# Kernel optimization log

Measured on AMD Instinct MI355X. Metric: run time of the kernel, lower is better.

The kernel has to match this reference:

```python
import jax, jax.numpy as jnp
import numpy as np
from jax import lax

NPOINT = 1024
NSAMPLE = 32
EPS = 1e-5


def setup_inputs() -> dict:
    key = jax.random.key(0)
    ks = jax.random.split(key, 8)
    B, N, CF = 16, 4096, 64
    xyz = jax.random.normal(ks[0], (B, N, 3), jnp.float32)
    points = jax.random.normal(ks[1], (B, N, CF), jnp.float32)
    in_ch = 3 + CF
    # 1x1 Conv2d weights stored as (out_ch, in_ch); kaiming-ish scale
    w0 = jax.random.normal(ks[2], (64, in_ch), jnp.float32) / np.sqrt(in_ch)
    w1 = jax.random.normal(ks[3], (64, 64), jnp.float32) / np.sqrt(64)
    w2 = jax.random.normal(ks[4], (128, 64), jnp.float32) / np.sqrt(64)
    z64 = jnp.zeros((64,), jnp.float32)
    z128 = jnp.zeros((128,), jnp.float32)
    o64 = jnp.ones((64,), jnp.float32)
    o128 = jnp.ones((128,), jnp.float32)
    return {
        "xyz": xyz, "points": points,
        "w0": w0, "b0": z64, "g0": o64, "bb0": z64,
        "w1": w1, "b1": z64, "g1": o64, "bb1": z64,
        "w2": w2, "b2": z128, "g2": o128, "bb2": z128,
    }


def _fps(xyz, npoint):
    """Iterative farthest point sampling. xyz: (B,N,3) -> (B,npoint) int32.
    Deterministic start at index 0 (torch uses a random start)."""
    B, N, _ = xyz.shape

    def step(carry, _):
        distance, farthest = carry
        centroid = jnp.take_along_axis(xyz, farthest[:, None, None], axis=1)  # (B,1,3)
        dist = jnp.sum((xyz - centroid) ** 2, -1)  # (B,N)
        distance = jnp.minimum(distance, dist)
        new_far = jnp.argmax(distance, axis=-1).astype(jnp.int32)
        return (distance, new_far), farthest

    init = (jnp.full((B, N), 1e10, xyz.dtype), jnp.zeros((B,), jnp.int32))
    _, cents = lax.scan(step, init, None, length=npoint)  # (npoint, B)
    return cents.T  # (B, npoint)


def _gather(pts, idx):
    """pts: (B,N,C), idx: (B,S,K) -> (B,S,K,C)"""
    return jax.vmap(lambda p, i: p[i])(pts, idx)


def _bn_relu(x, g, b):
    # training-mode BatchNorm over all axes except channel (last), biased var
    mean = jnp.mean(x, axis=(0, 1, 2))
    var = jnp.var(x, axis=(0, 1, 2))
    return jax.nn.relu(g * (x - mean) * lax.rsqrt(var + EPS) + b)


def reference(xyz, points, w0, b0, g0, bb0, w1, b1, g1, bb1, w2, b2, g2, bb2):
    B, N, _ = xyz.shape
    fps_idx = _fps(xyz, NPOINT)  # (B,S)
    new_xyz = jnp.take_along_axis(xyz, fps_idx[..., None], axis=1)  # (B,S,3)
    # squared distances centroid->all points: (B,S,N)
    d2 = (jnp.sum(new_xyz ** 2, -1)[:, :, None]
          + jnp.sum(xyz ** 2, -1)[:, None, :]
          - 2.0 * jnp.einsum("bsc,bnc->bsn", new_xyz, xyz))
    _, idx = lax.top_k(-d2, NSAMPLE)  # (B,S,K) nearest-K (sort-based ball query)
    grouped_xyz = _gather(xyz, idx) - new_xyz[:, :, None, :]  # (B,S,K,3)
    grouped_pts = _gather(points, idx)  # (B,S,K,CF)
    h = jnp.concatenate([grouped_xyz, grouped_pts], axis=-1)  # (B,S,K,3+CF)
    for w, b, g, bb in ((w0, b0, g0, bb0), (w1, b1, g1, bb1), (w2, b2, g2, bb2)):
        h = _bn_relu(jnp.einsum("bskc,oc->bsko", h, w) + b, g, bb)
    new_points = jnp.max(h, axis=2)  # (B,S,C_out) max over K
    new_points = jnp.transpose(new_points, (0, 2, 1))  # (B,C_out,S) matches torch
    return new_xyz, new_points
```

## Files before the change

kernel.cpp:

```cpp
#include <hip/hip_runtime.h>
#include <hip/hip_bf16.h>

#define NB 16
#define NN 4096
#define NS 1024
#define NK 32
#define CF 64
#define CIN 67
#define MTOT 524288
#define NEWP_OFF 49152

__device__ inline void stY(float* p, float v) { *p = v; }
__device__ inline void stY(__hip_bfloat16* p, float v) { *p = __float2bfloat16(v); }
__device__ inline float ldY(const float* p) { return *p; }
__device__ inline float ldY(const __hip_bfloat16* p) { return __bfloat162float(*p); }
__device__ inline float4 ldY4(const float* p) { return *(const float4*)p; }
__device__ inline float4 ldY4(const __hip_bfloat16* p) {
    return make_float4(ldY(p), ldY(p + 1), ldY(p + 2), ldY(p + 3));
}
__device__ inline void stY4(float* p, float4 v) { *(float4*)p = v; }
__device__ inline void stY4(__hip_bfloat16* p, float4 v) {
    stY(p, v.x); stY(p + 1, v.y); stY(p + 2, v.z); stY(p + 3, v.w);
}

template <int CTRL>
__device__ inline float dppredmax(float v) {
    int j = __builtin_amdgcn_update_dpp(__float_as_int(v), __float_as_int(v),
                                        CTRL, 0xF, 0xF, false);
    return fmaxf(v, __int_as_float(j));
}
template <int CTRL>
__device__ inline float dppredmin(float v) {
    int j = __builtin_amdgcn_update_dpp(__float_as_int(v), __float_as_int(v),
                                        CTRL, 0xF, 0xF, false);
    return fminf(v, __int_as_float(j));
}
template <int CTRL>
__device__ inline float dppadd0(float v) {
    int j = __builtin_amdgcn_update_dpp(0, __float_as_int(v), CTRL, 0xF, 0xF, true);
    return __fadd_rn(v, __int_as_float(j));
}
template <int CTRL>
__device__ inline unsigned long long dppredmin64(unsigned long long v) {
    int lo = (int)(unsigned)(v & 0xffffffffULL), hi = (int)(unsigned)(v >> 32);
    unsigned nlo = (unsigned)__builtin_amdgcn_update_dpp(lo, lo, CTRL, 0xF, 0xF, false);
    unsigned nhi = (unsigned)__builtin_amdgcn_update_dpp(hi, hi, CTRL, 0xF, 0xF, false);
    unsigned long long o = ((unsigned long long)nhi << 32) | nlo;
    return o < v ? o : v;
}
__device__ inline float wavemax_to_all(float tmax) {
    float g = tmax;
    g = dppredmax<0x111>(g);
    g = dppredmax<0x112>(g);
    g = dppredmax<0x114>(g);
    g = dppredmax<0x118>(g);
    g = dppredmax<0x142>(g);
    g = dppredmax<0x143>(g);
    return __int_as_float(__builtin_amdgcn_readlane(__float_as_int(g), 63));
}
__device__ inline unsigned long long wavemin64_to_all(unsigned long long v) {
    v = dppredmin64<0x111>(v);
    v = dppredmin64<0x112>(v);
    v = dppredmin64<0x114>(v);
    v = dppredmin64<0x118>(v);
    v = dppredmin64<0x142>(v);
    v = dppredmin64<0x143>(v);
    unsigned lo = (unsigned)__builtin_amdgcn_readlane((int)(unsigned)(v & 0xffffffffULL), 63);
    unsigned hi = (unsigned)__builtin_amdgcn_readlane((int)(unsigned)(v >> 32), 63);
    return ((unsigned long long)hi << 32) | lo;
}
__device__ inline float segsum16(float v) {
    v = dppadd0<0x111>(v); v = dppadd0<0x112>(v);
    v = dppadd0<0x114>(v); v = dppadd0<0x118>(v);
    return v;
}
__device__ inline float segsum32(float v) {
    v = segsum16(v); v = dppadd0<0x142>(v);
    return v;
}
__device__ inline float quadmax(float v) {
    v = dppredmax<0xB1>(v); v = dppredmax<0x4E>(v);
    return v;
}
__device__ inline float quadmin(float v) {
    v = dppredmin<0xB1>(v); v = dppredmin<0x4E>(v);
    return v;
}

__global__ __launch_bounds__(256) void fps_kernel(const float* __restrict__ xyz,
                                                  int* __restrict__ fps_idx) {
    __shared__ float4 cpt[NN];
    __shared__ unsigned long long part[2][4];
    const int b = blockIdx.x, t = threadIdx.x;
    const float4* src = (const float4*)(xyz + (size_t)b * NN * 3);
    float px[16], py[16], pz[16], dist[16];
#pragma unroll
    for (int j = 0; j < 4; ++j) {
        float4 A = src[t * 12 + 3 * j], B4 = src[t * 12 + 3 * j + 1], C4 = src[t * 12 + 3 * j + 2];
        px[4 * j + 0] = A.x;  py[4 * j + 0] = A.y;  pz[4 * j + 0] = A.z;
        px[4 * j + 1] = A.w;  py[4 * j + 1] = B4.x; pz[4 * j + 1] = B4.y;
        px[4 * j + 2] = B4.z; py[4 * j + 2] = B4.w; pz[4 * j + 2] = C4.x;
        px[4 * j + 3] = C4.y; py[4 * j + 3] = C4.z; pz[4 * j + 3] = C4.w;
    }
#pragma unroll
    for (int i = 0; i < 16; ++i) {
        dist[i] = 1e10f;
        cpt[16 * t + i] = make_float4(px[i], py[i], pz[i], 0.f);
    }
    __syncthreads();
    int cur = 0;
    float4 c = cpt[0];
    const int wv = t >> 6;
    for (int s = 0; s < NS; ++s) {
        if (t == 0) fps_idx[(b << 10) + s] = cur;
#pragma unroll
        for (int i = 0; i < 16; ++i) {
            float dx = __fsub_rn(px[i], c.x), dy = __fsub_rn(py[i], c.y), dz = __fsub_rn(pz[i], c.z);
            float d = __fadd_rn(__fadd_rn(__fmul_rn(dx, dx), __fmul_rn(dy, dy)), __fmul_rn(dz, dz));
            dist[i] = fminf(dist[i], d);
        }
        float m0 = fmaxf(dist[0], dist[1]),   m1 = fmaxf(dist[2], dist[3]);
        float m2 = fmaxf(dist[4], dist[5]),   m3 = fmaxf(dist[6], dist[7]);
        float m4 = fmaxf(dist[8], dist[9]),   m5 = fmaxf(dist[10], dist[11]);
        float m6 = fmaxf(dist[12], dist[13]), m7 = fmaxf(dist[14], dist[15]);
        m0 = fmaxf(m0, m1); m2 = fmaxf(m2, m3); m4 = fmaxf(m4, m5); m6 = fmaxf(m6, m7);
        m0 = fmaxf(m0, m2); m4 = fmaxf(m4, m6);
        const float tmax = fmaxf(m0, m4);
        int mi = 15;
#pragma unroll
        for (int i = 14; i >= 0; --i) mi = (dist[i] == tmax) ? i : mi;
        const float gmax = wavemax_to_all(tmax);
        unsigned long long mask = __ballot(tmax == gmax);
        int ldr = __ffsll(mask) - 1;
        int widx = __builtin_amdgcn_readlane(16 * t + mi, ldr);
        if ((t & 63) == 0) {
            part[s & 1][wv] =
                ((unsigned long long)__float_as_uint(gmax) << 32) | (unsigned)(4095 - widx);
        }
        __syncthreads();
        unsigned long long k0 = part[s & 1][0], k1 = part[s & 1][1];
        unsigned long long k2 = part[s & 1][2], k3 = part[s & 1][3];
        unsigned long long ka = k0 > k1 ? k0 : k1, kb = k2 > k3 ? k2 : k3;
        unsigned long long k = ka > kb ? ka : kb;
        cur = 4095 - (int)(unsigned)(k & 0xffffffffu);
        c = cpt[cur];
    }
}

__global__ __launch_bounds__(256) void knn_kernel(const float* __restrict__ xyz,
                                                  const int* __restrict__ fps_idx,
                                                  int* __restrict__ knn,
                                                  float* __restrict__ out) {
    __shared__ float4 cpt[NN];
    const int b = blockIdx.x >> 5, cb = blockIdx.x & 31, t = threadIdx.x;
    for (int p = t; p < NN; p += 256) {
        const float* xr = xyz + ((size_t)(b << 12) + p) * 3;
        float x = xr[0], y = xr[1], z = xr[2];
        float pn = __fadd_rn(__fadd_rn(__fmul_rn(x, x), __fmul_rn(y, y)), __fmul_rn(z, z));
        cpt[p] = make_float4(x, y, z, pn);
    }
    __syncthreads();
    const int lane = t & 63, wv = t >> 6;
    for (int r = 0; r < 8; ++r) {
        const int s = (cb << 5) + (wv << 3) + r;
        const int ci = fps_idx[(b << 10) + s];
        const float4 cq = cpt[ci];
        const float cx = cq.x, cy = cq.y, cz = cq.z, cn = cq.w;
        if (lane < 3) out[((size_t)(b << 10) + s) * 3 + lane] = (lane == 0) ? cx : (lane == 1 ? cy : cz);
        unsigned long long m1 = ~0ULL, m2 = ~0ULL, m3 = ~0ULL;
#pragma unroll
        for (int i = 0; i < 64; ++i) {
            int p = lane + (i << 6);
            float4 q = cpt[p];
            float dot = __fadd_rn(__fadd_rn(__fmul_rn(cx, q.x), __fmul_rn(cy, q.y)),
                                  __fmul_rn(cz, q.z));
            float d2 = __fsub_rn(__fadd_rn(cn, q.w), __fmul_rn(2.0f, dot));
            unsigned u = __float_as_uint(d2);
            unsigned enc = u ^ ((unsigned)((int)u >> 31) | 0x80000000u);
            unsigned long long key = ((unsigned long long)enc << 32) | (unsigned)p;
            if (key < m3) {
                if (key < m1)      { m3 = m2; m2 = m1; m1 = key; }
                else if (key < m2) { m3 = m2; m2 = key; }
                else               { m3 = key; }
            }
        }
        unsigned myidx = 0;
        for (int j = 0; j < 32; ++j) {
            const unsigned long long vmin = wavemin64_to_all(m1);
            if (lane == j) myidx = (unsigned)(vmin & 0xffffffffu);
            if (m1 == vmin) {
                m1 = m2; m2 = m3; m3 = ~0ULL;
                if (m1 == ~0ULL) {
#pragma unroll
                    for (int i = 0; i < 64; ++i) {
                        int p = lane + (i << 6);
                        float4 q = cpt[p];
                        float dot = __fadd_rn(__fadd_rn(__fmul_rn(cx, q.x), __fmul_rn(cy, q.y)),
                                              __fmul_rn(cz, q.z));
                        float d2 = __fsub_rn(__fadd_rn(cn, q.w), __fmul_rn(2.0f, dot));
                        unsigned u = __float_as_uint(d2);
                        unsigned enc = u ^ ((unsigned)((int)u >> 31) | 0x80000000u);
                        unsigned long long key = ((unsigned long long)enc << 32) | (unsigned)p;
                        if (key > vmin && key < m3) {
                            if (key < m1)      { m3 = m2; m2 = m1; m1 = key; }
                            else if (key < m2) { m3 = m2; m2 = key; }
                            else               { m3 = key; }
                        }
                    }
                }
            }
        }
        const int rowbase = ((b << 10) + s) << 5;
        if (lane < 32) knn[rowbase + lane] = (int)myidx;
    }
}

template <typename YT>
__global__ __launch_bounds__(256) void conv0_kernel(
    const float* __restrict__ xyz, const float* __restrict__ points,
    const float* __restrict__ out_xyz, const int* __restrict__ knn,
    const float* __restrict__ w0, const float* __restrict__ b0,
    YT* __restrict__ Y0, float* __restrict__ gs, float* __restrict__ gq) {
    __shared__ float Ht[CIN][128];
    __shared__ float Wt[CIN][64];
    __shared__ float bsm[64], bqm[64];
    const int t = threadIdx.x;
    const int eb = blockIdx.x << 7;
    for (int i = t; i < CIN * 64; i += 256) {
        int c = i >> 6, o = i & 63;
        Wt[c][o] = w0[o * CIN + c];
    }
    {
        const int le = t >> 1, part = t & 1;
        const int e = eb + le;
        const int b = e >> 15, s = (e >> 5) & 1023;
        const int pidx = knn[e];
        const float4* pr = (const float4*)(points + (((size_t)(b << 12) + pidx) << 6)) + (part << 3);
        if (part == 0) {
            const float* xr = xyz + ((size_t)(b << 12) + pidx) * 3;
            const float* cr = out_xyz + ((size_t)(b << 10) + s) * 3;
            Ht[0][le] = xr[0] - cr[0];
            Ht[1][le] = xr[1] - cr[1];
            Ht[2][le] = xr[2] - cr[2];
        }
#pragma unroll
        for (int q = 0; q < 8; ++q) {
            float4 v = pr[q];
            int c = 3 + (part << 5) + (q << 2);
            Ht[c][le] = v.x; Ht[c + 1][le] = v.y; Ht[c + 2][le] = v.z; Ht[c + 3][le] = v.w;
        }
    }
    __syncthreads();
    const int te = t & 31, to = t >> 5;
    float acc[4][8];
#pragma unroll
    for (int j = 0; j < 4; ++j)
#pragma unroll
        for (int i = 0; i < 8; ++i) acc[j][i] = 0.f;
#pragma unroll 2
    for (int c = 0; c < CIN; ++c) {
        const float4 a0 = *(const float4*)&Ht[c][te << 2];
        const float4 wa = *(const float4*)&Wt[c][to << 3];
        const float4 wb = *(const float4*)&Wt[c][(to << 3) + 4];
        const float av[4] = {a0.x, a0.y, a0.z, a0.w};
        const float wvv[8] = {wa.x, wa.y, wa.z, wa.w, wb.x, wb.y, wb.z, wb.w};
#pragma unroll
        for (int j = 0; j < 4; ++j)
#pragma unroll
            for (int i = 0; i < 8; ++i) acc[j][i] += av[j] * wvv[i];
    }
    const int o0 = to << 3;
    float s1v[8], s2v[8];
#pragma unroll
    for (int i = 0; i < 8; ++i) {
        const float bi = b0[o0 + i];
        float ss = 0.f, qq = 0.f;
#pragma unroll
        for (int j = 0; j < 4; ++j) {
            float v = acc[j][i] + bi;
            acc[j][i] = v;
            ss += v; qq += v * v;
        }
        s1v[i] = ss; s2v[i] = qq;
    }
#pragma unroll
    for (int i = 0; i < 8; ++i) {
        const size_t base = (size_t)(o0 + i) * MTOT + eb + (te << 2);
        stY4(&Y0[base], make_float4(acc[0][i], acc[1][i], acc[2][i], acc[3][i]));
    }
#pragma unroll
    for (int i = 0; i < 8; ++i) { s1v[i] = segsum32(s1v[i]); s2v[i] = segsum32(s2v[i]); }
    if ((t & 31) == 31) {
#pragma unroll
        for (int i = 0; i < 8; ++i) { bsm[o0 + i] = s1v[i]; bqm[o0 + i] = s2v[i]; }
    }
    __syncthreads();
    if (t < 64) atomicAdd(&gs[t], bsm[t]);
    else if (t < 128) atomicAdd(&gq[t - 64], bqm[t - 64]);
}

template <typename YT>
__global__ __launch_bounds__(256) void conv1_kernel(
    const YT* __restrict__ Y0, const float* __restrict__ w1, const float* __restrict__ b1,
    const float* __restrict__ gsp, const float* __restrict__ gqp,
    const float* __restrict__ g, const float* __restrict__ bb,
    YT* __restrict__ Y1, float* __restrict__ gs, float* __restrict__ gq) {
    __shared__ float At[64][128];
    __shared__ float Wt[64][64];
    __shared__ float bnsc[64], bnsh[64];
    __shared__ float bsm[64], bqm[64];
    const int t = threadIdx.x;
    const int eb = blockIdx.x << 7;
    if (t < 64) {
        const float inv = 1.f / (float)MTOT;
        float mean = gsp[t] * inv;
        float var = gqp[t] * inv - mean * mean;
        float r = g[t] / sqrtf(var + 1e-5f);
        bnsc[t] = r; bnsh[t] = bb[t] - mean * r;
    }
    for (int i = t; i < 4096; i += 256) {
        int c = i >> 6, o = i & 63;
        Wt[c][o] = w1[o * 64 + c];
    }
    __syncthreads();
#pragma unroll
    for (int r = 0; r < 8; ++r) {
        int L = (r << 8) + t;
        int c = L >> 5, col = (L & 31) << 2;
        float4 y = ldY4(&Y0[(size_t)c * MTOT + eb + col]);
        float sx = bnsc[c], hx = bnsh[c];
        At[c][col]     = fmaxf(sx * y.x + hx, 0.f);
        At[c][col + 1] = fmaxf(sx * y.y + hx, 0.f);
        At[c][col + 2] = fmaxf(sx * y.z + hx, 0.f);
        At[c][col + 3] = fmaxf(sx * y.w + hx, 0.f);
    }
    __syncthreads();
    const int te = t & 15, to = t >> 4;
    float acc[8][4];
#pragma unroll
    for (int j = 0; j < 8; ++j)
#pragma unroll
        for (int i = 0; i < 4; ++i) acc[j][i] = 0.f;
#pragma unroll 2
    for (int c = 0; c < 64; ++c) {
        const float4 a0 = *(const float4*)&At[c][te << 3];
        const float4 a1 = *(const float4*)&At[c][(te << 3) + 4];
        const float4 wa = *(const float4*)&Wt[c][to << 2];
        const float av[8] = {a0.x, a0.y, a0.z, a0.w, a1.x, a1.y, a1.z, a1.w};
        const float wvv[4] = {wa.x, wa.y, wa.z, wa.w};
#pragma unroll
        for (int j = 0; j < 8; ++j)
#pragma unroll
            for (int i = 0; i < 4; ++i) acc[j][i] += av[j] * wvv[i];
    }
    const int o0 = to << 2;
    float s1v[4], s2v[4];
#pragma unroll
    for (int i = 0; i < 4; ++i) {
        const float bi = b1[o0 + i];
        float ss = 0.f, qq = 0.f;
#pragma unroll
        for (int j = 0; j < 8; ++j) {
            float v = acc[j][i] + bi;
            acc[j][i] = v;
            ss += v; qq += v * v;
        }
        s1v[i] = ss; s2v[i] = qq;
    }
#pragma unroll
    for (int i = 0; i < 4; ++i) {
        const size_t base = (size_t)(o0 + i) * MTOT + eb + (te << 3);
        stY4(&Y1[base],     make_float4(acc[0][i], acc[1][i], acc[2][i], acc[3][i]));
        stY4(&Y1[base + 4], make_float4(acc[4][i], acc[5][i], acc[6][i], acc[7][i]));
    }
#pragma unroll
    for (int i = 0; i < 4; ++i) { s1v[i] = segsum16(s1v[i]); s2v[i] = segsum16(s2v[i]); }
    if ((t & 15) == 15) {
#pragma unroll
        for (int i = 0; i < 4; ++i) { bsm[o0 + i] = s1v[i]; bqm[o0 + i] = s2v[i]; }
    }
    __syncthreads();
    if (t < 64) atomicAdd(&gs[t], bsm[t]);
    else if (t < 128) atomicAdd(&gq[t - 64], bqm[t - 64]);
}

template <typename YT>
__global__ __launch_bounds__(256) void conv2s_kernel(
    const YT* __restrict__ Y1, const float* __restrict__ w2, const float* __restrict__ b2,
    const float* __restrict__ gsp, const float* __restrict__ gqp,
    const float* __restrict__ g, const float* __restrict__ bb,
    float* __restrict__ gs, float* __restrict__ gq,
    float* __restrict__ Mx, float* __restrict__ Mn) {
    __shared__ float At[64][128];
    __shared__ float Wt[64][128];
    __shared__ float bnsc[64], bnsh[64];
    __shared__ float bsm[128], bqm[128];
    __shared__ float mxs[4][128], mns[4][128];
    const int t = threadIdx.x;
    const int eb = blockIdx.x << 7;
    if (t < 64) {
        const float inv = 1.f / (float)MTOT;
        float mean = gsp[t] * inv;
        float var = gqp[t] * inv - mean * mean;
        float r = g[t] / sqrtf(var + 1e-5f);
        bnsc[t] = r; bnsh[t] = bb[t] - mean * r;
    }
    for (int i = t; i < 8192; i += 256) {
        int o = i & 127, c = i >> 7;
        Wt[c][o] = w2[o * 64 + c];
    }
    __syncthreads();
#pragma unroll
    for (int r = 0; r < 8; ++r) {
        int L = (r << 8) + t;
        int c = L >> 5, col = (L & 31) << 2;
        float4 y = ldY4(&Y1[(size_t)c * MTOT + eb + col]);
        float sx = bnsc[c], hx = bnsh[c];
        At[c][col]     = fmaxf(sx * y.x + hx, 0.f);
        At[c][col + 1] = fmaxf(sx * y.y + hx, 0.f);
        At[c][col + 2] = fmaxf(sx * y.z + hx, 0.f);
        At[c][col + 3] = fmaxf(sx * y.w + hx, 0.f);
    }
    __syncthreads();
    const int te = t & 15, to = t >> 4;
    float acc[8][8];
#pragma unroll
    for (int j = 0; j < 8; ++j)
#pragma unroll
        for (int i = 0; i < 8; ++i) acc[j][i] = 0.f;
#pragma unroll 2
    for (int c = 0; c < 64; ++c) {
        const float4 a0 = *(const float4*)&At[c][te << 3];
        const float4 a1 = *(const float4*)&At[c][(te << 3) + 4];
        const float4 wa = *(const float4*)&Wt[c][to << 3];
        const float4 wb = *(const float4*)&Wt[c][(to << 3) + 4];
        const float av[8] = {a0.x, a0.y, a0.z, a0.w, a1.x, a1.y, a1.z, a1.w};
        const float wvv[8] = {wa.x, wa.y, wa.z, wa.w, wb.x, wb.y, wb.z, wb.w};
#pragma unroll
        for (int j = 0; j < 8; ++j)
#pragma unroll
            for (int i = 0; i < 8; ++i) acc[j][i] += av[j] * wvv[i];
    }
    const int o0 = to << 3;
    float s1v[8], s2v[8], mxv[8], mnv[8];
#pragma unroll
    for (int i = 0; i < 8; ++i) {
        const float bi = b2[o0 + i];
        float ss = 0.f, qq = 0.f;
        float mx = -3.4e38f, mn = 3.4e38f;
#pragma unroll
        for (int j = 0; j < 8; ++j) {
            float v = acc[j][i] + bi;
            ss += v; qq += v * v;
            mx = fmaxf(mx, v); mn = fminf(mn, v);
        }
        s1v[i] = ss; s2v[i] = qq; mxv[i] = mx; mnv[i] = mn;
    }
#pragma unroll
    for (int i = 0; i < 8; ++i) {
        s1v[i] = segsum16(s1v[i]); s2v[i] = segsum16(s2v[i]);
        mxv[i] = quadmax(mxv[i]);  mnv[i] = quadmin(mnv[i]);
    }
    if ((t & 15) == 15) {
#pragma unroll
        for (int i = 0; i < 8; ++i) { bsm[o0 + i] = s1v[i]; bqm[o0 + i] = s2v[i]; }
    }
    if ((t & 3) == 0) {
        const int srow = (t & 15) >> 2;
#pragma unroll
        for (int i = 0; i < 8; ++i) { mxs[srow][o0 + i] = mxv[i]; mns[srow][o0 + i] = mnv[i]; }
    }
    __syncthreads();
    if (t < 128) atomicAdd(&gs[t], bsm[t]);
    else atomicAdd(&gq[t - 128], bqm[t - 128]);
    const int sidx0 = blockIdx.x << 2;
    for (int i = t; i < 512; i += 256) {
        int row = i >> 7, o = i & 127;
        Mx[(size_t)(sidx0 + row) * 128 + o] = mxs[row][o];
        Mn[(size_t)(sidx0 + row) * 128 + o] = mns[row][o];
    }
}

__global__ __launch_bounds__(256) void final2_kernel(
    const float* __restrict__ Mx, const float* __restrict__ Mn,
    const float* __restrict__ gsp, const float* __restrict__ gqp,
    const float* __restrict__ g, const float* __restrict__ bb,
    float* __restrict__ out) {
    __shared__ float T[128][65];
    __shared__ float bnsc[128], bnsh[128];
    const int t = threadIdx.x;
    if (t < 128) {
        const float inv = 1.f / (float)MTOT;
        float mean = gsp[t] * inv;
        float var = gqp[t] * inv - mean * mean;
        float r = g[t] / sqrtf(var + 1e-5f);
        bnsc[t] = r; bnsh[t] = bb[t] - mean * r;
    }
    __syncthreads();
    const int b = blockIdx.x >> 4, s0 = (blockIdx.x & 15) << 6;
    for (int i = t; i < 8192; i += 256) {
        int r = i >> 7, o = i & 127;
        size_t src = ((size_t)(b << 10) + s0 + r) * 128 + o;
        float a = bnsc[o];
        float m = (a >= 0.f) ? Mx[src] : Mn[src];
        T[o][r] = fmaxf(a * m + bnsh[o], 0.f);
    }
    __syncthreads();
    float* np = out + NEWP_OFF;
    for (int i = t; i < 8192; i += 256) {
        int o = i >> 6, r = i & 63;
        np[((size_t)(b << 7) + o) * 1024 + s0 + r] = T[o][r];
    }
}

extern "C" void kernel_launch(void* const* d_in, const int* in_sizes, int n_in,
                              void* d_out, int out_size, void* d_ws, size_t ws_size,
                              hipStream_t stream) {
    const float* xyz = (const float*)d_in[0];
    const float* points = (const float*)d_in[1];
    const float* w0 = (const float*)d_in[2];
    const float* b0 = (const float*)d_in[3];
    const float* g0 = (const float*)d_in[4];
    const float* bb0 = (const float*)d_in[5];
    const float* w1 = (const float*)d_in[6];
    const float* b1 = (const float*)d_in[7];
    const float* g1 = (const float*)d_in[8];
    const float* bb1 = (const float*)d_in[9];
    const float* w2 = (const float*)d_in[10];
    const float* b2 = (const float*)d_in[11];
    const float* g2 = (const float*)d_in[12];
    const float* bb2 = (const float*)d_in[13];
    float* out = (float*)d_out;
    char* ws = (char*)d_ws;

    int* knn = (int*)(ws);
    int* fps = (int*)(ws + (2u << 20));
    float* stats = (float*)(ws + (2u << 20) + (1u << 16));
    float *gs0 = stats, *gq0 = stats + 64, *gs1 = stats + 128, *gq1 = stats + 192;
    float *gs2 = stats + 256, *gq2 = stats + 384;
    float* Mx = (float*)(ws + (4ull << 20));
    float* Mn = (float*)(ws + (12ull << 20));
    const size_t yoff = 20ull << 20;
    const size_t ybytes_f32 = (size_t)MTOT * 64 * 4;
    const bool f32p = ws_size >= yoff + 2 * ybytes_f32;

    (void)hipMemsetAsync(stats, 0, 512 * sizeof(float), stream);
    fps_kernel<<<NB, 256, 0, stream>>>(xyz, fps);
    knn_kernel<<<NB * 32, 256, 0, stream>>>(xyz, fps, knn, out);

    if (f32p) {
        float* Y0 = (float*)(ws + yoff);
        float* Y1 = Y0 + (size_t)MTOT * 64;
        conv0_kernel<float><<<4096, 256, 0, stream>>>(xyz, points, out, knn, w0, b0, Y0, gs0, gq0);
        conv1_kernel<float><<<4096, 256, 0, stream>>>(Y0, w1, b1, gs0, gq0, g0, bb0, Y1, gs1, gq1);
        conv2s_kernel<float><<<4096, 256, 0, stream>>>(Y1, w2, b2, gs1, gq1, g1, bb1, gs2, gq2, Mx, Mn);
    } else {
        __hip_bfloat16* Y0 = (__hip_bfloat16*)(ws + yoff);
        __hip_bfloat16* Y1 = Y0 + (size_t)MTOT * 64;
        conv0_kernel<__hip_bfloat16><<<4096, 256, 0, stream>>>(xyz, points, out, knn, w0, b0, Y0, gs0, gq0);
        conv1_kernel<__hip_bfloat16><<<4096, 256, 0, stream>>>(Y0, w1, b1, gs0, gq0, g0, bb0, Y1, gs1, gq1);
        conv2s_kernel<__hip_bfloat16><<<4096, 256, 0, stream>>>(Y1, w2, b2, gs1, gq1, g1, bb1, gs2, gq2, Mx, Mn);
    }
    final2_kernel<<<256, 256, 0, stream>>>(Mx, Mn, gs2, gq2, g2, bb2, out);
}
```

Before: 1.286 ms.

## Use wave-uniform scalar weight loads in conv kernels instead of LDS weight tiles

The three conv kernels no longer stage transposed weights in shared memory. Each wave now owns a contiguous block of output channels and reads weights with wave-uniform indices straight from global memory, so they can be fetched as scalar loads. Each lane computes two elements, and the BN statistics and max/min are reduced with full-wave DPP sums. This frees LDS, drops the weight-staging pass and LDS weight reads, and vectorizes the activation staging writes. In exchange there is less register-level reuse per activation load, more scalar memory traffic, and narrower float2 stores to Y.

```diff
diff --git a/kernel.cpp b/kernel.cpp
--- a/kernel.cpp
+++ b/kernel.cpp
@@ -18,10 +18,8 @@
 __device__ inline float4 ldY4(const __hip_bfloat16* p) {
     return make_float4(ldY(p), ldY(p + 1), ldY(p + 2), ldY(p + 3));
 }
-__device__ inline void stY4(float* p, float4 v) { *(float4*)p = v; }
-__device__ inline void stY4(__hip_bfloat16* p, float4 v) {
-    stY(p, v.x); stY(p + 1, v.y); stY(p + 2, v.z); stY(p + 3, v.w);
-}
+__device__ inline void stY2(float* p, float a, float b) { *(float2*)p = make_float2(a, b); }
+__device__ inline void stY2(__hip_bfloat16* p, float a, float b) { stY(p, a); stY(p + 1, b); }
 
 template <int CTRL>
 __device__ inline float dppredmax(float v) {
@@ -69,21 +67,20 @@
     unsigned hi = (unsigned)__builtin_amdgcn_readlane((int)(unsigned)(v >> 32), 63);
     return ((unsigned long long)hi << 32) | lo;
 }
-__device__ inline float segsum16(float v) {
+__device__ inline float wavesum64(float v) {
     v = dppadd0<0x111>(v); v = dppadd0<0x112>(v);
     v = dppadd0<0x114>(v); v = dppadd0<0x118>(v);
+    v = dppadd0<0x142>(v); v = dppadd0<0x143>(v);
     return v;
 }
-__device__ inline float segsum32(float v) {
-    v = segsum16(v); v = dppadd0<0x142>(v);
+__device__ inline float segmax16(float v) {
+    v = dppredmax<0x111>(v); v = dppredmax<0x112>(v);
+    v = dppredmax<0x114>(v); v = dppredmax<0x118>(v);
     return v;
 }
-__device__ inline float quadmax(float v) {
-    v = dppredmax<0xB1>(v); v = dppredmax<0x4E>(v);
-    return v;
-}
-__device__ inline float quadmin(float v) {
-    v = dppredmin<0xB1>(v); v = dppredmin<0x4E>(v);
+__device__ inline float segmin16(float v) {
+    v = dppredmin<0x111>(v); v = dppredmin<0x112>(v);
+    v = dppredmin<0x114>(v); v = dppredmin<0x118>(v);
     return v;
 }
 
@@ -222,14 +219,9 @@
     const float* __restrict__ w0, const float* __restrict__ b0,
     YT* __restrict__ Y0, float* __restrict__ gs, float* __restrict__ gq) {
     __shared__ float Ht[CIN][128];
-    __shared__ float Wt[CIN][64];
     __shared__ float bsm[64], bqm[64];
     const int t = threadIdx.x;
     const int eb = blockIdx.x << 7;
-    for (int i = t; i < CIN * 64; i += 256) {
-        int c = i >> 6, o = i & 63;
-        Wt[c][o] = w0[o * CIN + c];
-    }
     {
         const int le = t >> 1, part = t & 1;
         const int e = eb + le;
@@ -251,48 +243,31 @@
         }
     }
     __syncthreads();
-    const int te = t & 31, to = t >> 5;
-    float acc[4][8];
-#pragma unroll
-    for (int j = 0; j < 4; ++j)
-#pragma unroll
-        for (int i = 0; i < 8; ++i) acc[j][i] = 0.f;
+    const int wvu = __builtin_amdgcn_readfirstlane(t >> 6);
+    const int lane = t & 63, e2 = (t & 63) << 1;
+    const float* __restrict__ wrow = w0 + (wvu << 4) * CIN;
+    float acc[16][2];
+#pragma unroll
+    for (int i = 0; i < 16; ++i) { acc[i][0] = 0.f; acc[i][1] = 0.f; }
 #pragma unroll 2
     for (int c = 0; c < CIN; ++c) {
-        const float4 a0 = *(const float4*)&Ht[c][te << 2];
-        const float4 wa = *(const float4*)&Wt[c][to << 3];
-        const float4 wb = *(const float4*)&Wt[c][(to << 3) + 4];
-        const float av[4] = {a0.x, a0.y, a0.z, a0.w};
-        const float wvv[8] = {wa.x, wa.y, wa.z, wa.w, wb.x, wb.y, wb.z, wb.w};
-#pragma unroll
-        for (int j = 0; j < 4; ++j)
-#pragma unroll
-            for (int i = 0; i < 8; ++i) acc[j][i] += av[j] * wvv[i];
-    }
-    const int o0 = to << 3;
-    float s1v[8], s2v[8];
-#pragma unroll
-    for (int i = 0; i < 8; ++i) {
+        const float2 a = *(const float2*)&Ht[c][e2];
+#pragma unroll
+        for (int i = 0; i < 16; ++i) {
+            const float w = wrow[i * CIN + c];
+            acc[i][0] += w * a.x;
+            acc[i][1] += w * a.y;
+        }
+    }
+    const int o0 = wvu << 4;
+#pragma unroll
+    for (int i = 0; i < 16; ++i) {
         const float bi = b0[o0 + i];
-        float ss = 0.f, qq = 0.f;
-#pragma unroll
-        for (int j = 0; j < 4; ++j) {
-            float v = acc[j][i] + bi;
-            acc[j][i] = v;
-            ss += v; qq += v * v;
-        }
-        s1v[i] = ss; s2v[i] = qq;
-    }
-#pragma unroll
-    for (int i = 0; i < 8; ++i) {
-        const size_t base = (size_t)(o0 + i) * MTOT + eb + (te << 2);
-        stY4(&Y0[base], make_float4(acc[0][i], acc[1][i], acc[2][i], acc[3][i]));
-    }
-#pragma unroll
-    for (int i = 0; i < 8; ++i) { s1v[i] = segsum32(s1v[i]); s2v[i] = segsum32(s2v[i]); }
-    if ((t & 31) == 31) {
-#pragma unroll
-        for (int i = 0; i < 8; ++i) { bsm[o0 + i] = s1v[i]; bqm[o0 + i] = s2v[i]; }
+        const float v0 = acc[i][0] + bi, v1 = acc[i][1] + bi;
+        stY2(&Y0[(size_t)(o0 + i) * MTOT + eb + e2], v0, v1);
+        float ss = wavesum64(v0 + v1);
+        float qq = wavesum64(v0 * v0 + v1 * v1);
+        if (lane == 63) { bsm[o0 + i] = ss; bqm[o0 + i] = qq; }
     }
     __syncthreads();
     if (t < 64) atomicAdd(&gs[t], bsm[t]);
@@ -306,7 +281,6 @@
     const float* __restrict__ g, const float* __restrict__ bb,
     YT* __restrict__ Y1, float* __restrict__ gs, float* __restrict__ gq) {
     __shared__ float At[64][128];
-    __shared__ float Wt[64][64];
     __shared__ float bnsc[64], bnsh[64];
     __shared__ float bsm[64], bqm[64];
     const int t = threadIdx.x;
@@ -318,66 +292,46 @@
         float r = g[t] / sqrtf(var + 1e-5f);
         bnsc[t] = r; bnsh[t] = bb[t] - mean * r;
     }
-    for (int i = t; i < 4096; i += 256) {
-        int c = i >> 6, o = i & 63;
-        Wt[c][o] = w1[o * 64 + c];
-    }
-    __syncthreads();
-#pragma unroll
-    for (int r = 0; r < 8; ++r) {
-        int L = (r << 8) + t;
-        int c = L >> 5, col = (L & 31) << 2;
-        float4 y = ldY4(&Y0[(size_t)c * MTOT + eb + col]);
-        float sx = bnsc[c], hx = bnsh[c];
-        At[c][col]     = fmaxf(sx * y.x + hx, 0.f);
-        At[c][col + 1] = fmaxf(sx * y.y + hx, 0.f);
-        At[c][col + 2] = fmaxf(sx * y.z + hx, 0.f);
-        At[c][col + 3] = fmaxf(sx * y.w + hx, 0.f);
-    }
-    __syncthreads();
-    const int te = t & 15, to = t >> 4;
-    float acc[8][4];
-#pragma unroll
-    for (int j = 0; j < 8; ++j)
-#pragma unroll
-        for (int i = 0; i < 4; ++i) acc[j][i] = 0.f;
+    __syncthreads();
+    {
+        const int c = t >> 2, base = (t & 3) << 5;
+        const float sx = bnsc[c], hx = bnsh[c];
+#pragma unroll
+        for (int q = 0; q < 8; ++q) {
+            const int col = base + (q << 2);
+            float4 y = ldY4(&Y0[(size_t)c * MTOT + eb + col]);
+            *(float4*)&At[c][col] = make_float4(fmaxf(sx * y.x + hx, 0.f),
+                                                fmaxf(sx * y.y + hx, 0.f),
+                                                fmaxf(sx * y.z + hx, 0.f),
+                                                fmaxf(sx * y.w + hx, 0.f));
+        }
+    }
+    __syncthreads();
+    const int wvu = __builtin_amdgcn_readfirstlane(t >> 6);
+    const int lane = t & 63, e2 = (t & 63) << 1;
+    const float* __restrict__ wrow = w1 + (wvu << 4) * 64;
+    float acc[16][2];
+#pragma unroll
+    for (int i = 0; i < 16; ++i) { acc[i][0] = 0.f; acc[i][1] = 0.f; }
 #pragma unroll 2
     for (int c = 0; c < 64; ++c) {
-        const float4 a0 = *(const float4*)&At[c][te << 3];
-        const float4 a1 = *(const float4*)&At[c][(te << 3) + 4];
-        const float4 wa = *(const float4*)&Wt[c][to << 2];
-        const float av[8] = {a0.x, a0.y, a0.z, a0.w, a1.x, a1.y, a1.z, a1.w};
-        const float wvv[4] = {wa.x, wa.y, wa.z, wa.w};
-#pragma unroll
-        for (int j = 0; j < 8; ++j)
-#pragma unroll
-            for (int i = 0; i < 4; ++i) acc[j][i] += av[j] * wvv[i];
-    }
-    const int o0 = to << 2;
-    float s1v[4], s2v[4];
-#pragma unroll
-    for (int i = 0; i < 4; ++i) {
+        const float2 a = *(const float2*)&At[c][e2];
+#pragma unroll
+        for (int i = 0; i < 16; ++i) {
+            const float w = wrow[(i << 6) + c];
+            acc[i][0] += w * a.x;
+            acc[i][1] += w * a.y;
+        }
+    }
+    const int o0 = wvu << 4;
+#pragma unroll
+    for (int i = 0; i < 16; ++i) {
         const float bi = b1[o0 + i];
-        float ss = 0.f, qq = 0.f;
-#pragma unroll
-        for (int j = 0; j < 8; ++j) {
-            float v = acc[j][i] + bi;
-            acc[j][i] = v;
-            ss += v; qq += v * v;
-        }
-        s1v[i] = ss; s2v[i] = qq;
-    }
-#pragma unroll
-    for (int i = 0; i < 4; ++i) {
-        const size_t base = (size_t)(o0 + i) * MTOT + eb + (te << 3);
-        stY4(&Y1[base],     make_float4(acc[0][i], acc[1][i], acc[2][i], acc[3][i]));
-        stY4(&Y1[base + 4], make_float4(acc[4][i], acc[5][i], acc[6][i], acc[7][i]));
-    }
-#pragma unroll
-    for (int i = 0; i < 4; ++i) { s1v[i] = segsum16(s1v[i]); s2v[i] = segsum16(s2v[i]); }
-    if ((t & 15) == 15) {
-#pragma unroll
-        for (int i = 0; i < 4; ++i) { bsm[o0 + i] = s1v[i]; bqm[o0 + i] = s2v[i]; }
+        const float v0 = acc[i][0] + bi, v1 = acc[i][1] + bi;
+        stY2(&Y1[(size_t)(o0 + i) * MTOT + eb + e2], v0, v1);
+        float ss = wavesum64(v0 + v1);
+        float qq = wavesum64(v0 * v0 + v1 * v1);
+        if (lane == 63) { bsm[o0 + i] = ss; bqm[o0 + i] = qq; }
     }
     __syncthreads();
     if (t < 64) atomicAdd(&gs[t], bsm[t]);
@@ -392,7 +346,6 @@
     float* __restrict__ gs, float* __restrict__ gq,
     float* __restrict__ Mx, float* __restrict__ Mn) {
     __shared__ float At[64][128];
-    __shared__ float Wt[64][128];
     __shared__ float bnsc[64], bnsh[64];
     __shared__ float bsm[128], bqm[128];
     __shared__ float mxs[4][128], mns[4][128];
@@ -405,70 +358,49 @@
         float r = g[t] / sqrtf(var + 1e-5f);
         bnsc[t] = r; bnsh[t] = bb[t] - mean * r;
     }
-    for (int i = t; i < 8192; i += 256) {
-        int o = i & 127, c = i >> 7;
-        Wt[c][o] = w2[o * 64 + c];
-    }
-    __syncthreads();
-#pragma unroll
-    for (int r = 0; r < 8; ++r) {
-        int L = (r << 8) + t;
-        int c = L >> 5, col = (L & 31) << 2;
-        float4 y = ldY4(&Y1[(size_t)c * MTOT + eb + col]);
-        float sx = bnsc[c], hx = bnsh[c];
-        At[c][col]     = fmaxf(sx * y.x + hx, 0.f);
-        At[c][col + 1] = fmaxf(sx * y.y + hx, 0.f);
-        At[c][col + 2] = fmaxf(sx * y.z + hx, 0.f);
-        At[c][col + 3] = fmaxf(sx * y.w + hx, 0.f);
-    }
-    __syncthreads();
-    const int te = t & 15, to = t >> 4;
-    float acc[8][8];
-#pragma unroll
-    for (int j = 0; j < 8; ++j)
-#pragma unroll
-        for (int i = 0; i < 8; ++i) acc[j][i] = 0.f;
+    __syncthreads();
+    {
+        const int c = t >> 2, base = (t & 3) << 5;
+        const float sx = bnsc[c], hx = bnsh[c];
+#pragma unroll
+        for (int q = 0; q < 8; ++q) {
+            const int col = base + (q << 2);
+            float4 y = ldY4(&Y1[(size_t)c * MTOT + eb + col]);
+            *(float4*)&At[c][col] = make_float4(fmaxf(sx * y.x + hx, 0.f),
+                                                fmaxf(sx * y.y + hx, 0.f),
+                                                fmaxf(sx * y.z + hx, 0.f),
+                                                fmaxf(sx * y.w + hx, 0.f));
+        }
+    }
+    __syncthreads();
+    const int wvu = __builtin_amdgcn_readfirstlane(t >> 6);
+    const int lane = t & 63, e2 = (t & 63) << 1;
+    const float* __restrict__ wrow = w2 + (wvu << 5) * 64;
+    float acc[32][2];
+#pragma unroll
+    for (int i = 0; i < 32; ++i) { acc[i][0] = 0.f; acc[i][1] = 0.f; }
 #pragma unroll 2
     for (int c = 0; c < 64; ++c) {
-        const float4 a0 = *(const float4*)&At[c][te << 3];
-        const float4 a1 = *(const float4*)&At[c][(te << 3) + 4];
-        const float4 wa = *(const float4*)&Wt[c][to << 3];
-        const float4 wb = *(const float4*)&Wt[c][(to << 3) + 4];
-        const float av[8] = {a0.x, a0.y, a0.z, a0.w, a1.x, a1.y, a1.z, a1.w};
-        const float wvv[8] = {wa.x, wa.y, wa.z, wa.w, wb.x, wb.y, wb.z, wb.w};
-#pragma unroll
-        for (int j = 0; j < 8; ++j)
-#pragma unroll
-            for (int i = 0; i < 8; ++i) acc[j][i] += av[j] * wvv[i];
-    }
-    const int o0 = to << 3;
-    float s1v[8], s2v[8], mxv[8], mnv[8];
-#pragma unroll
-    for (int i = 0; i < 8; ++i) {
+        const float2 a = *(const float2*)&At[c][e2];
+#pragma unroll
+        for (int i = 0; i < 32; ++i) {
+            const float w = wrow[(i << 6) + c];
+            acc[i][0] += w * a.x;
+            acc[i][1] += w * a.y;
+        }
+    }
+    const int o0 = wvu << 5;
+    const int srow = lane >> 4;
+#pragma unroll
+    for (int i = 0; i < 32; ++i) {
         const float bi = b2[o0 + i];
-        float ss = 0.f, qq = 0.f;
-        float mx = -3.4e38f, mn = 3.4e38f;
-#pragma unroll
-        for (int j = 0; j < 8; ++j) {
-            float v = acc[j][i] + bi;
-            ss += v; qq += v * v;
-            mx = fmaxf(mx, v); mn = fminf(mn, v);
-        }
-        s1v[i] = ss; s2v[i] = qq; mxv[i] = mx; mnv[i] = mn;
-    }
-#pragma unroll
-    for (int i = 0; i < 8; ++i) {
-        s1v[i] = segsum16(s1v[i]); s2v[i] = segsum16(s2v[i]);
-        mxv[i] = quadmax(mxv[i]);  mnv[i] = quadmin(mnv[i]);
-    }
-    if ((t & 15) == 15) {
-#pragma unroll
-        for (int i = 0; i < 8; ++i) { bsm[o0 + i] = s1v[i]; bqm[o0 + i] = s2v[i]; }
-    }
-    if ((t & 3) == 0) {
-        const int srow = (t & 15) >> 2;
-#pragma unroll
-        for (int i = 0; i < 8; ++i) { mxs[srow][o0 + i] = mxv[i]; mns[srow][o0 + i] = mnv[i]; }
+        const float v0 = acc[i][0] + bi, v1 = acc[i][1] + bi;
+        float ss = wavesum64(v0 + v1);
+        float qq = wavesum64(v0 * v0 + v1 * v1);
+        if (lane == 63) { bsm[o0 + i] = ss; bqm[o0 + i] = qq; }
+        float mx = segmax16(fmaxf(v0, v1));
+        float mn = segmin16(fminf(v0, v1));
+        if ((lane & 15) == 15) { mxs[srow][o0 + i] = mx; mns[srow][o0 + i] = mn; }
     }
     __syncthreads();
     if (t < 128) atomicAdd(&gs[t], bsm[t]);
```

Measured after the change: 1.306 ms. About the same (+1.5%).
